# Kernel optimization log

Measured on AMD Instinct MI355X. Metric: run time of the kernel, lower is better.

## Reference

```python
import jax, jax.numpy as jnp
import numpy as np

DIM_H = 384
EPS = 0.5
HID = 768
NN = 3   # num_normal_labels (B,I,O)
NL = 7   # num_labels (O, B/I x POS/NEG/NEU)


def _make_w_trans():
    # ote_vocab: B=0, I=1, O=2 ; ts_vocab: O=0, B-POS=1, B-NEG=2, B-NEU=3, I-POS=4, I-NEG=5, I-NEU=6
    W = np.zeros((NN, NL), dtype=np.float32)
    W[0, 1] = W[0, 2] = W[0, 3] = 1.0 / 3.0  # B -> B-*
    W[1, 4] = W[1, 5] = W[1, 6] = 1.0 / 3.0  # I -> I-*
    W[2, 0] = 1.0                            # O -> O
    return jnp.asarray(W)


def setup_inputs() -> dict:
    key = jax.random.key(0)
    ks = jax.random.split(key, 16)
    B, S = 32, 512
    s = 0.02
    inp = {
        'x': jax.random.normal(ks[0], (B, S, HID), jnp.float32),
        'attention_mask': jnp.ones((B, S), jnp.int32),
        'labels': jax.random.randint(ks[1], (B, S), 0, NL, jnp.int32),
        'labels_normal': jax.random.randint(ks[2], (B, S), 0, NN, jnp.int32),
        'W_fc_normal': jax.random.normal(ks[3], (HID, NN), jnp.float32) * s,
        'b_fc_normal': jnp.zeros((NN,), jnp.float32),
        'w_ih_f': jax.random.normal(ks[4], (4 * DIM_H, HID), jnp.float32) * s,
        'w_hh_f': jax.random.normal(ks[5], (4 * DIM_H, DIM_H), jnp.float32) * s,
        'b_f': jnp.zeros((4 * DIM_H,), jnp.float32),
        'w_ih_b': jax.random.normal(ks[6], (4 * DIM_H, HID), jnp.float32) * s,
        'w_hh_b': jax.random.normal(ks[7], (4 * DIM_H, DIM_H), jnp.float32) * s,
        'b_b': jnp.zeros((4 * DIM_H,), jnp.float32),
        'W_gate': jax.random.uniform(ks[8], (2 * DIM_H, 2 * DIM_H), jnp.float32, -0.2, 0.2),
        'W_fc_upper': jax.random.normal(ks[9], (2 * DIM_H, NL), jnp.float32) * s,
        'b_fc_upper': jnp.zeros((NL,), jnp.float32),
        'W_trans': _make_w_trans(),
    }
    return inp


def _lstm_dir(xs, w_ih, w_hh, b):
    # xs: [S, B, HID] time-major; PyTorch gate order i,f,g,o
    B = xs.shape[1]
    pre = jnp.einsum('sbh,gh->sbg', xs, w_ih) + b  # precompute input projections

    def step(carry, p_t):
        h, c = carry
        g = p_t + h @ w_hh.T
        i, f, gg, o = jnp.split(g, 4, axis=-1)
        c = jax.nn.sigmoid(f) * c + jax.nn.sigmoid(i) * jnp.tanh(gg)
        h = jax.nn.sigmoid(o) * jnp.tanh(c)
        return (h, c), h

    init = (jnp.zeros((B, DIM_H), xs.dtype), jnp.zeros((B, DIM_H), xs.dtype))
    _, hs = jax.lax.scan(step, init, pre)
    return hs  # [S, B, DIM_H]


def _masked_ce(logits, labels, mask):
    logp = jax.nn.log_softmax(logits, axis=-1)
    nll = -jnp.take_along_axis(logp, labels[..., None].astype(jnp.int32), axis=-1)[..., 0]
    m = mask.astype(logits.dtype)
    return jnp.sum(nll * m) / jnp.sum(m)


def reference(x, attention_mask, labels, labels_normal, W_fc_normal, b_fc_normal,
              w_ih_f, w_hh_f, b_f, w_ih_b, w_hh_b, b_b, W_gate,
              W_fc_upper, b_fc_upper, W_trans):
    z_t = x @ W_fc_normal + b_fc_normal                      # [B,S,NN]
    loss = _masked_ce(z_t, labels_normal, attention_mask)

    xs = jnp.transpose(x, (1, 0, 2))                         # [S,B,HID]
    hf = _lstm_dir(xs, w_ih_f, w_hh_f, b_f)
    hb = _lstm_dir(xs[::-1], w_ih_b, w_hh_b, b_b)[::-1]
    h_s = jnp.concatenate([hf, hb], axis=-1)                 # [S,B,2*DIM_H]

    # gated highway recurrence: gates depend only on h_s -> batched matmul + linear scan
    g = jax.nn.sigmoid(h_s @ W_gate)                         # [S,B,768]

    def gate_step(h_prev, inp):
        ht, gt = inp
        h = gt * ht + (1.0 - gt) * h_prev
        return h, h

    _, rest = jax.lax.scan(gate_step, h_s[0], (h_s[1:], g[1:]))
    h_tilde = jnp.concatenate([h_s[:1], rest], axis=0)       # [S,B,768]
    h_tilde = jnp.transpose(h_tilde, (1, 0, 2))              # [B,S,768]; dropout = identity (eval)

    z_s = h_tilde @ W_fc_upper + b_fc_upper                  # [B,S,NL]
    p = jax.nn.softmax(z_t, axis=-1)
    alpha = EPS * jnp.sum(p * p, axis=-1, keepdims=True)     # [B,S,1]
    z_s_prime = z_t @ W_trans                                # [B,S,NL]
    z_s_tilde = z_s_prime * alpha + z_s * (1.0 - alpha)

    loss = loss + _masked_ce(z_s_tilde, labels, attention_mask)
    return loss, z_s_tilde
```

## Files before the change

### kernel.cpp

```cpp
#include <hip/hip_runtime.h>

#define B_SZ   32
#define S_LEN  512
#define HID    768
#define DH     384
#define G4     1536
#define NPOS   16384
#define EPS_C  0.5f
#define NCH    24576
#define CHK    64
#define NCHK   8

typedef _Float16 h2 __attribute__((ext_vector_type(2)));
typedef short bf16x8 __attribute__((ext_vector_type(8)));
typedef float f32x4 __attribute__((ext_vector_type(4)));

static __device__ __forceinline__ float sigm(float x) { return 1.0f / (1.0f + __expf(-x)); }
static __device__ __forceinline__ float tanh_fast(float x) {
    return 1.0f - 2.0f / (__expf(2.0f * x) + 1.0f);
}

static __device__ __forceinline__ unsigned short f2bf(float f) {
    union { float f; unsigned u; } v; v.f = f;
    unsigned r = v.u + 0x7FFF + ((v.u >> 16) & 1);
    return (unsigned short)(r >> 16);
}
static __device__ __forceinline__ float bf2f(unsigned short u) {
    union { unsigned u; float f; } v; v.u = ((unsigned)u) << 16; return v.f;
}

static __device__ __forceinline__ float wred(float v) {
#pragma unroll
    for (int off = 32; off > 0; off >>= 1) v += __shfl_down(v, off, 64);
    return v;
}

static __device__ __forceinline__ float dot2acc(h2 a, h2 b, float c) {
#if __has_builtin(__builtin_amdgcn_fdot2)
    return __builtin_amdgcn_fdot2(a, b, c, false);
#else
    return c + (float)a.x * (float)b.x + (float)a.y * (float)b.y;
#endif
}

static __device__ __forceinline__ h2 hcast(unsigned u) { return __builtin_bit_cast(h2, u); }

template <int CTRL>
static __device__ __forceinline__ float dpp_shl_add(float v) {
#if __has_builtin(__builtin_amdgcn_mov_dpp)
    int o = __builtin_amdgcn_mov_dpp(__builtin_bit_cast(int, v), CTRL, 0xF, 0xF, true);
    return v + __builtin_bit_cast(float, o);
#else
    return v + __shfl_down(v, CTRL - 0x100, 64);
#endif
}
static __device__ __forceinline__ float red8(float v) {
    v = dpp_shl_add<0x101>(v);
    v = dpp_shl_add<0x102>(v);
    v = dpp_shl_add<0x104>(v);
    return v;
}

__global__ void wprep(const float* __restrict__ wf, const float* __restrict__ wb,
                      unsigned* __restrict__ wpk) {
    int gid = blockIdx.x * 256 + threadIdx.x;
    int d = (gid >= 294912) ? 1 : 0;
    int j = gid - d * 294912;
    const float* src = d ? wb : wf;
    _Float16 a = (_Float16)src[2 * j];
    _Float16 b = (_Float16)src[2 * j + 1];
    unsigned pa = __builtin_bit_cast(unsigned short, a);
    unsigned pb = __builtin_bit_cast(unsigned short, b);
    wpk[(size_t)d * 294912 + j] = pa | (pb << 16);
}

__global__ __launch_bounds__(256) void cast_bf16(
    const float* __restrict__ src, unsigned short* __restrict__ dst, int n4) {
    int i = blockIdx.x * 256 + threadIdx.x;
    if (i >= n4) return;
    float4 v = *(const float4*)(src + (size_t)i * 4);
    ushort4 o;
    o.x = f2bf(v.x); o.y = f2bf(v.y); o.z = f2bf(v.z); o.w = f2bf(v.w);
    *(ushort4*)(dst + (size_t)i * 4) = o;
}

__global__ __launch_bounds__(256) void wgt_prep(
    const float* __restrict__ Wg, unsigned short* __restrict__ Wgt) {
    int i = blockIdx.x * 256 + threadIdx.x;
    int k = i / 768, n = i - k * 768;
    Wgt[(size_t)n * 768 + k] = f2bf(Wg[i]);
}

__global__ __launch_bounds__(256) void zt_kernel(
    const float* __restrict__ x, const int* __restrict__ amask,
    const int* __restrict__ labn, const float* __restrict__ Wfc,
    const float* __restrict__ bfc, const float* __restrict__ Wtr,
    float* __restrict__ alpha, float* __restrict__ zsp,
    float* __restrict__ p0, float* __restrict__ p2) {
    const int gid  = blockIdx.x * blockDim.x + threadIdx.x;
    const int pos  = gid >> 6, lane = gid & 63, wv = threadIdx.x >> 6;
    __shared__ float r0[4], r2[4];
    const float* xp = x + (size_t)pos * HID;
    float a0 = 0.f, a1 = 0.f, a2 = 0.f;
#pragma unroll
    for (int j = 0; j < 12; ++j) {
        int k = lane + (j << 6);
        float xv = xp[k];
        a0 += xv * Wfc[k * 3 + 0];
        a1 += xv * Wfc[k * 3 + 1];
        a2 += xv * Wfc[k * 3 + 2];
    }
    a0 = wred(a0); a1 = wred(a1); a2 = wred(a2);
    if (lane == 0) {
        float z0 = a0 + bfc[0], z1 = a1 + bfc[1], z2 = a2 + bfc[2];
        float mx = fmaxf(z0, fmaxf(z1, z2));
        float e0 = __expf(z0 - mx), e1 = __expf(z1 - mx), e2 = __expf(z2 - mx);
        float se = e0 + e1 + e2;
        float m  = (float)amask[pos];
        int  lab = labn[pos];
        float zl = (lab == 0) ? z0 : ((lab == 1) ? z1 : z2);
        r0[wv] = (mx + __logf(se) - zl) * m;
        r2[wv] = m;
        float q0 = e0 / se, q1 = e1 / se, q2 = e2 / se;
        alpha[pos] = EPS_C * (q0 * q0 + q1 * q1 + q2 * q2);
#pragma unroll
        for (int cc = 0; cc < 7; ++cc)
            zsp[(size_t)pos * 7 + cc] = z0 * Wtr[cc] + z1 * Wtr[7 + cc] + z2 * Wtr[14 + cc];
    }
    __syncthreads();
    if (threadIdx.x == 0) {
        p0[blockIdx.x] = r0[0] + r0[1] + r0[2] + r0[3];
        p2[blockIdx.x] = r2[0] + r2[1] + r2[2] + r2[3];
    }
}

__global__ __launch_bounds__(256) void gemm_mfma(
    const unsigned short* __restrict__ A, const unsigned short* __restrict__ B,
    const float* __restrict__ bias, void* __restrict__ Cout,
    int M, int N, int K, int mode) {
    __shared__ __align__(16) unsigned short As[128][40];
    __shared__ __align__(16) unsigned short Bs[128][40];
    const int tid = threadIdx.x;
    const int m0 = blockIdx.y * 128, n0 = blockIdx.x * 128;
    const int wave = tid >> 6, lane = tid & 63;
    const int wm = (wave & 1) * 64, wn = (wave >> 1) * 64;
    const int lm = lane & 15, quad = lane >> 4;
    f32x4 acc[4][4] = {};

    for (int k0 = 0; k0 < K; k0 += 32) {
#pragma unroll
        for (int r = 0; r < 2; ++r) {
            int seg = tid + r * 256;
            int row = seg >> 2, c16 = (seg & 3) << 3;
            uint4 va = *(const uint4*)(A + (size_t)(m0 + row) * K + k0 + c16);
            *(uint4*)&As[row][c16] = va;
            uint4 vb = *(const uint4*)(B + (size_t)(n0 + row) * K + k0 + c16);
            *(uint4*)&Bs[row][c16] = vb;
        }
        __syncthreads();
        bf16x8 af[4], bfr[4];
#pragma unroll
        for (int i = 0; i < 4; ++i) {
            af[i]  = *(const bf16x8*)&As[wm + i * 16 + lm][quad * 8];
            bfr[i] = *(const bf16x8*)&Bs[wn + i * 16 + lm][quad * 8];
        }
#pragma unroll
        for (int mi = 0; mi < 4; ++mi)
#pragma unroll
            for (int ni = 0; ni < 4; ++ni)
                acc[mi][ni] = __builtin_amdgcn_mfma_f32_16x16x32_bf16(
                    af[mi], bfr[ni], acc[mi][ni], 0, 0, 0);
        __syncthreads();
    }

    const int rbase = quad * 4;
#pragma unroll
    for (int mi = 0; mi < 4; ++mi) {
#pragma unroll
        for (int ni = 0; ni < 4; ++ni) {
            const int col = n0 + wn + ni * 16 + lm;
            const float bv = (mode == 0) ? bias[col] : 0.0f;
#pragma unroll
            for (int r = 0; r < 4; ++r) {
                const int row = m0 + wm + mi * 16 + rbase + r;
                float v = acc[mi][ni][r];
                if (mode == 0)
                    ((unsigned short*)Cout)[(size_t)row * N + col] = f2bf(v + bv);
                else
                    ((unsigned short*)Cout)[(size_t)row * N + col] = f2bf(sigm(v));
            }
        }
    }
}

#define DOT8(W, H, A0, A1) { \
    A0 = dot2acc(hcast(W.x), hcast(H.x), A0); \
    A1 = dot2acc(hcast(W.y), hcast(H.y), A1); \
    A0 = dot2acc(hcast(W.z), hcast(H.z), A0); \
    A1 = dot2acc(hcast(W.w), hcast(H.w), A1); }

__global__ __launch_bounds__(768)
__attribute__((amdgpu_waves_per_eu(3, 3)))
void lstm_scan10(
    const unsigned* __restrict__ wpk,
    const unsigned short* __restrict__ pre,
    unsigned short* __restrict__ h_sb,
    unsigned long long* __restrict__ hx64) {
    const int blk   = blockIdx.x;
    const int chain = blk & 63;
    const int rp    = blk >> 6;
    const int d = chain >> 5, b = chain & 31;
    const int tid = threadIdx.x;
    const int u = tid >> 3;
    const int p = tid & 7;
    const int base = rp * 96;
    const int G0 = base + u;

    __shared__ __align__(16) _Float16 lh16[2][384];

    const uint4* wq = (const uint4*)wpk + ((size_t)d * 1536 + G0) * 48 + p * 6;
    const uint4 wi0 = wq[0],         wi1 = wq[1],         wi2 = wq[2],
                wi3 = wq[3],         wi4 = wq[4],         wi5 = wq[5];
    const uint4 wf0 = wq[18432],     wf1 = wq[18433],     wf2 = wq[18434],
                wf3 = wq[18435],     wf4 = wq[18436],     wf5 = wq[18437];
    const uint4 wg0 = wq[36864],     wg1 = wq[36865],     wg2 = wq[36866],
                wg3 = wq[36867],     wg4 = wq[36868],     wg5 = wq[36869];
    const uint4 wo0 = wq[55296],     wo1 = wq[55297],     wo2 = wq[55298],
                wo3 = wq[55299],     wo4 = wq[55300],     wo5 = wq[55301];

    const unsigned short* prb =
        pre + ((size_t)d * B_SZ + b) * S_LEN * G4 + G0 + (p & 3) * 384;

    float c = 0.0f;

    for (int s = 0; s < S_LEN; ++s) {
        const int t  = d ? (S_LEN - 1 - s) : s;
        const int lb = s & 1;
        float prev = 0.0f;
        if (p < 4) prev = bf2f(prb[(size_t)t * G4]);

        if (s == 0) {
            if (tid < 384) lh16[0][tid] = (_Float16)0.0f;
        } else if (tid < 288) {
            const int uu = tid + (tid >= base ? 96 : 0);
            const unsigned long long* srcp =
                hx64 + ((size_t)((s - 1) & 1) * 64 + chain) * 384 + uu;
            unsigned long long v =
                __hip_atomic_load(srcp, __ATOMIC_RELAXED, __HIP_MEMORY_SCOPE_AGENT);
            while ((unsigned)(v >> 32) != (unsigned)(s - 1)) {
                __builtin_amdgcn_s_sleep(1);
                v = __hip_atomic_load(srcp, __ATOMIC_RELAXED, __HIP_MEMORY_SCOPE_AGENT);
            }
            lh16[lb][uu] = (_Float16)__builtin_bit_cast(float, (unsigned)v);
        }
        __syncthreads();

        {
            const uint4* hq = (const uint4*)&lh16[lb][0] + p * 6;
            const uint4 h0 = hq[0], h1 = hq[1], h2 = hq[2],
                        h3 = hq[3], h4 = hq[4], h5 = hq[5];
            float i0 = 0.f, i1 = 0.f, f0 = 0.f, f1 = 0.f;
            float g0 = 0.f, g1 = 0.f, o0 = 0.f, o1 = 0.f;
            DOT8(wi0, h0, i0, i1) DOT8(wi1, h1, i0, i1) DOT8(wi2, h2, i0, i1)
            DOT8(wi3, h3, i0, i1) DOT8(wi4, h4, i0, i1) DOT8(wi5, h5, i0, i1)
            DOT8(wf0, h0, f0, f1) DOT8(wf1, h1, f0, f1) DOT8(wf2, h2, f0, f1)
            DOT8(wf3, h3, f0, f1) DOT8(wf4, h4, f0, f1) DOT8(wf5, h5, f0, f1)
            DOT8(wg0, h0, g0, g1) DOT8(wg1, h1, g0, g1) DOT8(wg2, h2, g0, g1)
            DOT8(wg3, h3, g0, g1) DOT8(wg4, h4, g0, g1) DOT8(wg5, h5, g0, g1)
            DOT8(wo0, h0, o0, o1) DOT8(wo1, h1, o0, o1) DOT8(wo2, h2, o0, o1)
            DOT8(wo3, h3, o0, o1) DOT8(wo4, h4, o0, o1) DOT8(wo5, h5, o0, o1)
            float gi = i0 + i1, gf = f0 + f1, gg = g0 + g1, go = o0 + o1;
            if      (p == 0) gi += prev;
            else if (p == 1) gf += prev;
            else if (p == 2) gg += prev;
            else if (p == 3) go += prev;
            gi = red8(gi); gf = red8(gf); gg = red8(gg); go = red8(go);

            if (p == 0) {
                c = sigm(gf) * c + sigm(gi) * tanh_fast(gg);
                float h = sigm(go) * tanh_fast(c);
                unsigned long long v = ((unsigned long long)(unsigned)s << 32)
                                     | (unsigned long long)__builtin_bit_cast(unsigned, h);
                __hip_atomic_store(hx64 + ((size_t)lb * 64 + chain) * 384 + G0,
                                   v, __ATOMIC_RELAXED, __HIP_MEMORY_SCOPE_AGENT);
                h_sb[((size_t)t * B_SZ + b) * HID + d * DH + G0] = f2bf(h);
                lh16[lb ^ 1][G0] = (_Float16)h;
            }
        }
    }
}

__global__ __launch_bounds__(256) void gscanA(
    const unsigned short* __restrict__ g, const unsigned short* __restrict__ hsb,
    float2* __restrict__ ab) {
    int id = blockIdx.x * 256 + threadIdx.x;
    int chunk = id / NCH, chain = id - chunk * NCH;
    int t0 = chunk * CHK;
    float A = 1.f, Bv = 0.f;
    for (int i = 0; i < CHK; ++i) {
        int t = t0 + i;
        size_t idx = (size_t)t * NCH + chain;
        float gv = bf2f(g[idx]);
        float hv = bf2f(hsb[idx]);
        float a = (t == 0) ? 0.f : (1.f - gv);
        float bb = (t == 0) ? hv : gv * hv;
        A  = a * A;
        Bv = a * Bv + bb;
    }
    ab[id] = make_float2(A, Bv);
}

__global__ __launch_bounds__(256) void gscanB(
    const float2* __restrict__ ab, float* __restrict__ cin) {
    int chain = blockIdx.x * 256 + threadIdx.x;
    float h = 0.f;
#pragma unroll
    for (int j = 0; j < NCHK; ++j) {
        cin[(size_t)j * NCH + chain] = h;
        float2 t = ab[(size_t)j * NCH + chain];
        h = t.x * h + t.y;
    }
}

__global__ __launch_bounds__(256) void gscanC(
    const unsigned short* __restrict__ g, unsigned short* __restrict__ hsb,
    const float* __restrict__ cin) {
    int id = blockIdx.x * 256 + threadIdx.x;
    int chunk = id / NCH, chain = id - chunk * NCH;
    int t0 = chunk * CHK;
    float h = cin[(size_t)chunk * NCH + chain];
    for (int i = 0; i < CHK; ++i) {
        int t = t0 + i;
        size_t idx = (size_t)t * NCH + chain;
        float gv = bf2f(g[idx]);
        float v  = bf2f(hsb[idx]);
        h = (t == 0) ? v : (gv * v + (1.f - gv) * h);
        hsb[idx] = f2bf(h);
    }
}

__global__ __launch_bounds__(256) void final_k(
    const unsigned short* __restrict__ ht, const float* __restrict__ Wup,
    const float* __restrict__ bup, const float* __restrict__ alpha,
    const float* __restrict__ zsp, const int* __restrict__ labels,
    const int* __restrict__ amask, float* __restrict__ out, float* __restrict__ p1) {
    const int gid = blockIdx.x * blockDim.x + threadIdx.x;
    const int pos = gid >> 6, lane = gid & 63, wv = threadIdx.x >> 6;
    __shared__ float r1[4];
    const int bb = pos >> 9, tt = pos & 511;
    const unsigned short* hp = ht + (size_t)tt * (B_SZ * HID) + (size_t)bb * HID;
    float acc[7] = {};
#pragma unroll
    for (int j = 0; j < 12; ++j) {
        int k = lane + (j << 6);
        float hv = bf2f(hp[k]);
        const float* wr = Wup + k * 7;
#pragma unroll
        for (int cc = 0; cc < 7; ++cc) acc[cc] += hv * wr[cc];
    }
#pragma unroll
    for (int cc = 0; cc < 7; ++cc) acc[cc] = wred(acc[cc]);
    if (lane == 0) {
        float al = alpha[pos];
        float z[7], mx = -1e30f;
#pragma unroll
        for (int cc = 0; cc < 7; ++cc) {
            float v = acc[cc] + bup[cc];
            v = zsp[(size_t)pos * 7 + cc] * al + v * (1.0f - al);
            z[cc] = v;
            mx = fmaxf(mx, v);
            out[1 + (size_t)pos * 7 + cc] = v;
        }
        float se = 0.f;
#pragma unroll
        for (int cc = 0; cc < 7; ++cc) se += __expf(z[cc] - mx);
        float lse = mx + __logf(se);
        int lab = labels[pos];
        float zl = z[0];
#pragma unroll
        for (int cc = 1; cc < 7; ++cc) if (lab == cc) zl = z[cc];
        float m = (float)amask[pos];
        r1[wv] = (lse - zl) * m;
    }
    __syncthreads();
    if (threadIdx.x == 0)
        p1[blockIdx.x] = r1[0] + r1[1] + r1[2] + r1[3];
}

__global__ __launch_bounds__(256) void loss_k(
    const float* __restrict__ p0, const float* __restrict__ p1,
    const float* __restrict__ p2, float* __restrict__ out) {
    const int tid = threadIdx.x, lane = tid & 63, wv = tid >> 6;
    __shared__ float rs[4][3];
    float s0 = 0.f, s1 = 0.f, s2 = 0.f;
    for (int i = tid; i < 4096; i += 256) {
        s0 += p0[i]; s1 += p1[i]; s2 += p2[i];
    }
    s0 = wred(s0); s1 = wred(s1); s2 = wred(s2);
    if (lane == 0) { rs[wv][0] = s0; rs[wv][1] = s1; rs[wv][2] = s2; }
    __syncthreads();
    if (tid == 0) {
        float t0 = rs[0][0] + rs[1][0] + rs[2][0] + rs[3][0];
        float t1 = rs[0][1] + rs[1][1] + rs[2][1] + rs[3][1];
        float t2 = rs[0][2] + rs[1][2] + rs[2][2] + rs[3][2];
        out[0] = t0 / t2 + t1 / t2;
    }
}

extern "C" void kernel_launch(void* const* d_in, const int* in_sizes, int n_in,
                              void* d_out, int out_size, void* d_ws, size_t ws_size,
                              hipStream_t stream) {
    const float* x     = (const float*)d_in[0];
    const int*   amask = (const int*)d_in[1];
    const int*   labels= (const int*)d_in[2];
    const int*   labn  = (const int*)d_in[3];
    const float* Wfc   = (const float*)d_in[4];
    const float* bfc   = (const float*)d_in[5];
    const float* wihf  = (const float*)d_in[6];
    const float* whhf  = (const float*)d_in[7];
    const float* bf    = (const float*)d_in[8];
    const float* wihb  = (const float*)d_in[9];
    const float* whhb  = (const float*)d_in[10];
    const float* bb    = (const float*)d_in[11];
    const float* Wg    = (const float*)d_in[12];
    const float* Wup   = (const float*)d_in[13];
    const float* bup   = (const float*)d_in[14];
    const float* Wtr   = (const float*)d_in[15];
    float* out = (float*)d_out;
    (void)in_sizes; (void)n_in; (void)out_size; (void)ws_size;

    char* ws = (char*)d_ws;
    size_t off = 0;
    auto alloc = [&](size_t bytes) -> char* {
        char* p = ws + off;
        off = (off + bytes + 255) & ~(size_t)255;
        return p;
    };
    unsigned* w16buf    = (unsigned*)alloc((size_t)2 * 1536 * 192 * 4);
    unsigned short* pre = (unsigned short*)alloc((size_t)2 * NPOS * G4 * 2);
    unsigned short* xb  = (unsigned short*)alloc((size_t)NPOS * HID * 2);
    unsigned short* wfb = (unsigned short*)alloc((size_t)G4 * HID * 2);
    unsigned short* wbb = (unsigned short*)alloc((size_t)G4 * HID * 2);
    unsigned short* wgt = (unsigned short*)alloc((size_t)HID * HID * 2);
    float* alpha        = (float*)alloc((size_t)NPOS * 4);
    float* zsp          = (float*)alloc((size_t)NPOS * 7 * 4);
    unsigned long long* hx64 = (unsigned long long*)alloc((size_t)2 * 64 * 384 * 8);
    float2* ab          = (float2*)alloc((size_t)NCHK * NCH * 8);
    float* cin          = (float*)alloc((size_t)NCHK * NCH * 4);
    float* part0        = (float*)alloc(4096 * 4);
    float* part1        = (float*)alloc(4096 * 4);
    float* part2        = (float*)alloc(4096 * 4);
    unsigned short* gbuf = (unsigned short*)pre;
    unsigned short* h_sb = xb;


    wprep<<<2304, 256, 0, stream>>>(whhf, whhb, w16buf);
    cast_bf16<<<12288, 256, 0, stream>>>(x, xb, NPOS * HID / 4);
    cast_bf16<<<1152, 256, 0, stream>>>(wihf, wfb, G4 * HID / 4);
    cast_bf16<<<1152, 256, 0, stream>>>(wihb, wbb, G4 * HID / 4);
    wgt_prep<<<2304, 256, 0, stream>>>(Wg, wgt);

    zt_kernel<<<4096, 256, 0, stream>>>(x, amask, labn, Wfc, bfc, Wtr, alpha, zsp,
                                        part0, part2);

    gemm_mfma<<<dim3(12, 128), 256, 0, stream>>>(xb, wfb, bf, pre, NPOS, G4, HID, 0);
    gemm_mfma<<<dim3(12, 128), 256, 0, stream>>>(xb, wbb, bb, pre + (size_t)NPOS * G4,
                                                 NPOS, G4, HID, 0);

    lstm_scan10<<<256, 768, 0, stream>>>(w16buf, pre, h_sb, hx64);

    gemm_mfma<<<dim3(6, 128), 256, 0, stream>>>(h_sb, wgt, nullptr, gbuf, NPOS, HID, HID, 1);

    gscanA<<<768, 256, 0, stream>>>(gbuf, h_sb, ab);
    gscanB<<<96, 256, 0, stream>>>(ab, cin);
    gscanC<<<768, 256, 0, stream>>>(gbuf, h_sb, cin);

    final_k<<<4096, 256, 0, stream>>>(h_sb, Wup, bup, alpha, zsp, labels, amask, out, part1);

    loss_k<<<1, 256, 0, stream>>>(part0, part1, part2, out);
}
```

Before: 1.376 ms.

## Process two batch chains per LSTM scan block to reuse register-held weights

Each persistent LSTM scan block now handles two batch chains (b and b+16) in the same direction, so the recurrent weights held in registers serve two hidden-state dot products per step. The grid shrinks from 256 to 128 blocks, and all 768 threads take part in the hidden-state exchange and pre-activation loads. This halves the number of blocks spinning on cross-block flags and doubles arithmetic per weight load. In exchange, each step does twice the serial dot-product work per block, which may lengthen the per-step critical path.

```diff
diff --git a/kernel.cpp b/kernel.cpp
--- a/kernel.cpp
+++ b/kernel.cpp
@@ -201,22 +201,25 @@
 
 __global__ __launch_bounds__(768)
 __attribute__((amdgpu_waves_per_eu(3, 3)))
-void lstm_scan10(
+void lstm_scan11(
     const unsigned* __restrict__ wpk,
     const unsigned short* __restrict__ pre,
     unsigned short* __restrict__ h_sb,
     unsigned long long* __restrict__ hx64) {
-    const int blk   = blockIdx.x;
-    const int chain = blk & 63;
-    const int rp    = blk >> 6;
-    const int d = chain >> 5, b = chain & 31;
+    const int blk  = blockIdx.x;
+    const int pair = blk & 31;
+    const int rp   = blk >> 5;
+    const int d  = pair >> 4;
+    const int bb = pair & 15;
+    const int b0 = bb, b1 = bb + 16;
+    const int c0 = d * 32 + b0, c1 = d * 32 + b1;
     const int tid = threadIdx.x;
     const int u = tid >> 3;
     const int p = tid & 7;
     const int base = rp * 96;
     const int G0 = base + u;
 
-    __shared__ __align__(16) _Float16 lh16[2][384];
+    __shared__ __align__(16) _Float16 lh16[2][2][384];
 
     const uint4* wq = (const uint4*)wpk + ((size_t)d * 1536 + G0) * 48 + p * 6;
     const uint4 wi0 = wq[0],         wi1 = wq[1],         wi2 = wq[2],
@@ -228,64 +231,98 @@
     const uint4 wo0 = wq[55296],     wo1 = wq[55297],     wo2 = wq[55298],
                 wo3 = wq[55299],     wo4 = wq[55300],     wo5 = wq[55301];
 
+    const int pb = (p < 4) ? b0 : b1;
     const unsigned short* prb =
-        pre + ((size_t)d * B_SZ + b) * S_LEN * G4 + G0 + (p & 3) * 384;
-
-    float c = 0.0f;
+        pre + ((size_t)d * B_SZ + pb) * S_LEN * G4 + G0 + (p & 3) * 384;
+
+    const int sc = (tid >= 384) ? 1 : 0;
+    const int st = tid - sc * 384;
+    const int sch = sc ? c1 : c0;
+
+    float cs0 = 0.0f, cs1 = 0.0f;
 
     for (int s = 0; s < S_LEN; ++s) {
         const int t  = d ? (S_LEN - 1 - s) : s;
         const int lb = s & 1;
-        float prev = 0.0f;
-        if (p < 4) prev = bf2f(prb[(size_t)t * G4]);
+        float prev = bf2f(prb[(size_t)t * G4]);
 
         if (s == 0) {
-            if (tid < 384) lh16[0][tid] = (_Float16)0.0f;
-        } else if (tid < 288) {
-            const int uu = tid + (tid >= base ? 96 : 0);
+            lh16[0][sc][st] = (_Float16)0.0f;
+        } else if (st < 288) {
+            const int uu = st + (st >= base ? 96 : 0);
             const unsigned long long* srcp =
-                hx64 + ((size_t)((s - 1) & 1) * 64 + chain) * 384 + uu;
+                hx64 + ((size_t)((s - 1) & 1) * 64 + sch) * 384 + uu;
             unsigned long long v =
                 __hip_atomic_load(srcp, __ATOMIC_RELAXED, __HIP_MEMORY_SCOPE_AGENT);
             while ((unsigned)(v >> 32) != (unsigned)(s - 1)) {
                 __builtin_amdgcn_s_sleep(1);
                 v = __hip_atomic_load(srcp, __ATOMIC_RELAXED, __HIP_MEMORY_SCOPE_AGENT);
             }
-            lh16[lb][uu] = (_Float16)__builtin_bit_cast(float, (unsigned)v);
+            lh16[lb][sc][uu] = (_Float16)__builtin_bit_cast(float, (unsigned)v);
         }
         __syncthreads();
 
+        float gi0, gf0, gg0, go0, gi1, gf1, gg1, go1;
         {
-            const uint4* hq = (const uint4*)&lh16[lb][0] + p * 6;
-            const uint4 h0 = hq[0], h1 = hq[1], h2 = hq[2],
-                        h3 = hq[3], h4 = hq[4], h5 = hq[5];
+            const uint4* hq0 = (const uint4*)&lh16[lb][0][0] + p * 6;
+            const uint4 h00 = hq0[0], h01 = hq0[1], h02 = hq0[2],
+                        h03 = hq0[3], h04 = hq0[4], h05 = hq0[5];
             float i0 = 0.f, i1 = 0.f, f0 = 0.f, f1 = 0.f;
             float g0 = 0.f, g1 = 0.f, o0 = 0.f, o1 = 0.f;
-            DOT8(wi0, h0, i0, i1) DOT8(wi1, h1, i0, i1) DOT8(wi2, h2, i0, i1)
-            DOT8(wi3, h3, i0, i1) DOT8(wi4, h4, i0, i1) DOT8(wi5, h5, i0, i1)
-            DOT8(wf0, h0, f0, f1) DOT8(wf1, h1, f0, f1) DOT8(wf2, h2, f0, f1)
-            DOT8(wf3, h3, f0, f1) DOT8(wf4, h4, f0, f1) DOT8(wf5, h5, f0, f1)
-            DOT8(wg0, h0, g0, g1) DOT8(wg1, h1, g0, g1) DOT8(wg2, h2, g0, g1)
-            DOT8(wg3, h3, g0, g1) DOT8(wg4, h4, g0, g1) DOT8(wg5, h5, g0, g1)
-            DOT8(wo0, h0, o0, o1) DOT8(wo1, h1, o0, o1) DOT8(wo2, h2, o0, o1)
-            DOT8(wo3, h3, o0, o1) DOT8(wo4, h4, o0, o1) DOT8(wo5, h5, o0, o1)
-            float gi = i0 + i1, gf = f0 + f1, gg = g0 + g1, go = o0 + o1;
-            if      (p == 0) gi += prev;
-            else if (p == 1) gf += prev;
-            else if (p == 2) gg += prev;
-            else if (p == 3) go += prev;
-            gi = red8(gi); gf = red8(gf); gg = red8(gg); go = red8(go);
-
-            if (p == 0) {
-                c = sigm(gf) * c + sigm(gi) * tanh_fast(gg);
-                float h = sigm(go) * tanh_fast(c);
-                unsigned long long v = ((unsigned long long)(unsigned)s << 32)
-                                     | (unsigned long long)__builtin_bit_cast(unsigned, h);
-                __hip_atomic_store(hx64 + ((size_t)lb * 64 + chain) * 384 + G0,
-                                   v, __ATOMIC_RELAXED, __HIP_MEMORY_SCOPE_AGENT);
-                h_sb[((size_t)t * B_SZ + b) * HID + d * DH + G0] = f2bf(h);
-                lh16[lb ^ 1][G0] = (_Float16)h;
-            }
+            DOT8(wi0, h00, i0, i1) DOT8(wi1, h01, i0, i1) DOT8(wi2, h02, i0, i1)
+            DOT8(wi3, h03, i0, i1) DOT8(wi4, h04, i0, i1) DOT8(wi5, h05, i0, i1)
+            DOT8(wf0, h00, f0, f1) DOT8(wf1, h01, f0, f1) DOT8(wf2, h02, f0, f1)
+            DOT8(wf3, h03, f0, f1) DOT8(wf4, h04, f0, f1) DOT8(wf5, h05, f0, f1)
+            DOT8(wg0, h00, g0, g1) DOT8(wg1, h01, g0, g1) DOT8(wg2, h02, g0, g1)
+            DOT8(wg3, h03, g0, g1) DOT8(wg4, h04, g0, g1) DOT8(wg5, h05, g0, g1)
+            DOT8(wo0, h00, o0, o1) DOT8(wo1, h01, o0, o1) DOT8(wo2, h02, o0, o1)
+            DOT8(wo3, h03, o0, o1) DOT8(wo4, h04, o0, o1) DOT8(wo5, h05, o0, o1)
+            gi0 = i0 + i1; gf0 = f0 + f1; gg0 = g0 + g1; go0 = o0 + o1;
+        }
+        {
+            const uint4* hq1 = (const uint4*)&lh16[lb][1][0] + p * 6;
+            const uint4 h10 = hq1[0], h11 = hq1[1], h12 = hq1[2],
+                        h13 = hq1[3], h14 = hq1[4], h15 = hq1[5];
+            float i0 = 0.f, i1 = 0.f, f0 = 0.f, f1 = 0.f;
+            float g0 = 0.f, g1 = 0.f, o0 = 0.f, o1 = 0.f;
+            DOT8(wi0, h10, i0, i1) DOT8(wi1, h11, i0, i1) DOT8(wi2, h12, i0, i1)
+            DOT8(wi3, h13, i0, i1) DOT8(wi4, h14, i0, i1) DOT8(wi5, h15, i0, i1)
+            DOT8(wf0, h10, f0, f1) DOT8(wf1, h11, f0, f1) DOT8(wf2, h12, f0, f1)
+            DOT8(wf3, h13, f0, f1) DOT8(wf4, h14, f0, f1) DOT8(wf5, h15, f0, f1)
+            DOT8(wg0, h10, g0, g1) DOT8(wg1, h11, g0, g1) DOT8(wg2, h12, g0, g1)
+            DOT8(wg3, h13, g0, g1) DOT8(wg4, h14, g0, g1) DOT8(wg5, h15, g0, g1)
+            DOT8(wo0, h10, o0, o1) DOT8(wo1, h11, o0, o1) DOT8(wo2, h12, o0, o1)
+            DOT8(wo3, h13, o0, o1) DOT8(wo4, h14, o0, o1) DOT8(wo5, h15, o0, o1)
+            gi1 = i0 + i1; gf1 = f0 + f1; gg1 = g0 + g1; go1 = o0 + o1;
+        }
+        if      (p == 0) gi0 += prev;
+        else if (p == 1) gf0 += prev;
+        else if (p == 2) gg0 += prev;
+        else if (p == 3) go0 += prev;
+        else if (p == 4) gi1 += prev;
+        else if (p == 5) gf1 += prev;
+        else if (p == 6) gg1 += prev;
+        else             go1 += prev;
+        gi0 = red8(gi0); gf0 = red8(gf0); gg0 = red8(gg0); go0 = red8(go0);
+        gi1 = red8(gi1); gf1 = red8(gf1); gg1 = red8(gg1); go1 = red8(go1);
+
+        if (p == 0) {
+            cs0 = sigm(gf0) * cs0 + sigm(gi0) * tanh_fast(gg0);
+            float h0 = sigm(go0) * tanh_fast(cs0);
+            cs1 = sigm(gf1) * cs1 + sigm(gi1) * tanh_fast(gg1);
+            float h1 = sigm(go1) * tanh_fast(cs1);
+            unsigned long long v0 = ((unsigned long long)(unsigned)s << 32)
+                                  | (unsigned long long)__builtin_bit_cast(unsigned, h0);
+            unsigned long long v1 = ((unsigned long long)(unsigned)s << 32)
+                                  | (unsigned long long)__builtin_bit_cast(unsigned, h1);
+            __hip_atomic_store(hx64 + ((size_t)lb * 64 + c0) * 384 + G0,
+                               v0, __ATOMIC_RELAXED, __HIP_MEMORY_SCOPE_AGENT);
+            __hip_atomic_store(hx64 + ((size_t)lb * 64 + c1) * 384 + G0,
+                               v1, __ATOMIC_RELAXED, __HIP_MEMORY_SCOPE_AGENT);
+            h_sb[((size_t)t * B_SZ + b0) * HID + d * DH + G0] = f2bf(h0);
+            h_sb[((size_t)t * B_SZ + b1) * HID + d * DH + G0] = f2bf(h1);
+            lh16[lb ^ 1][0][G0] = (_Float16)h0;
+            lh16[lb ^ 1][1][G0] = (_Float16)h1;
         }
     }
 }
@@ -467,7 +504,7 @@
     gemm_mfma<<<dim3(12, 128), 256, 0, stream>>>(xb, wbb, bb, pre + (size_t)NPOS * G4,
                                                  NPOS, G4, HID, 0);
 
-    lstm_scan10<<<256, 768, 0, stream>>>(w16buf, pre, h_sb, hx64);
+    lstm_scan11<<<128, 768, 0, stream>>>(w16buf, pre, h_sb, hx64);
 
     gemm_mfma<<<dim3(6, 128), 256, 0, stream>>>(h_sb, wgt, nullptr, gbuf, NPOS, HID, HID, 1);
 
```

Measured after the change: 2.092 ms. +52.0%, slower.

## Move half of LSTM recurrent weights to LDS and fuse x cast into zt_kernel

Applied to the files above, without the earlier changes.

The persistent LSTM scan kernel used to keep all four gate weight slices in registers. Now it keeps only the i and f slices there and stages the g and o slices in dynamic shared memory (about 148 KB), reading them back from LDS on every timestep. This cuts register pressure, at the price of extra LDS traffic inside the latency-critical recurrence loop. Separately, the bf16 cast of x is folded into zt_kernel, which already reads x, so one full pass over the input and one kernel launch are removed.

```diff
diff --git a/kernel.cpp b/kernel.cpp
--- a/kernel.cpp
+++ b/kernel.cpp
@@ -96,16 +96,19 @@
     const int* __restrict__ labn, const float* __restrict__ Wfc,
     const float* __restrict__ bfc, const float* __restrict__ Wtr,
     float* __restrict__ alpha, float* __restrict__ zsp,
-    float* __restrict__ p0, float* __restrict__ p2) {
+    float* __restrict__ p0, float* __restrict__ p2,
+    unsigned short* __restrict__ xb) {
     const int gid  = blockIdx.x * blockDim.x + threadIdx.x;
     const int pos  = gid >> 6, lane = gid & 63, wv = threadIdx.x >> 6;
     __shared__ float r0[4], r2[4];
     const float* xp = x + (size_t)pos * HID;
+    unsigned short* xo = xb + (size_t)pos * HID;
     float a0 = 0.f, a1 = 0.f, a2 = 0.f;
 #pragma unroll
     for (int j = 0; j < 12; ++j) {
         int k = lane + (j << 6);
         float xv = xp[k];
+        xo[k] = f2bf(xv);
         a0 += xv * Wfc[k * 3 + 0];
         a1 += xv * Wfc[k * 3 + 1];
         a2 += xv * Wfc[k * 3 + 2];
@@ -201,7 +204,7 @@
 
 __global__ __launch_bounds__(768)
 __attribute__((amdgpu_waves_per_eu(3, 3)))
-void lstm_scan10(
+void lstm_scan12(
     const unsigned* __restrict__ wpk,
     const unsigned short* __restrict__ pre,
     unsigned short* __restrict__ h_sb,
@@ -216,17 +219,21 @@
     const int base = rp * 96;
     const int G0 = base + u;
 
-    __shared__ __align__(16) _Float16 lh16[2][384];
+    extern __shared__ __align__(16) char smem[];
+    uint4*     wlds = (uint4*)smem;
+    _Float16*  lh16 = (_Float16*)(smem + 12 * 768 * 16);
 
     const uint4* wq = (const uint4*)wpk + ((size_t)d * 1536 + G0) * 48 + p * 6;
-    const uint4 wi0 = wq[0],         wi1 = wq[1],         wi2 = wq[2],
-                wi3 = wq[3],         wi4 = wq[4],         wi5 = wq[5];
-    const uint4 wf0 = wq[18432],     wf1 = wq[18433],     wf2 = wq[18434],
-                wf3 = wq[18435],     wf4 = wq[18436],     wf5 = wq[18437];
-    const uint4 wg0 = wq[36864],     wg1 = wq[36865],     wg2 = wq[36866],
-                wg3 = wq[36867],     wg4 = wq[36868],     wg5 = wq[36869];
-    const uint4 wo0 = wq[55296],     wo1 = wq[55297],     wo2 = wq[55298],
-                wo3 = wq[55299],     wo4 = wq[55300],     wo5 = wq[55301];
+    const uint4 wi0 = wq[0],     wi1 = wq[1],     wi2 = wq[2],
+                wi3 = wq[3],     wi4 = wq[4],     wi5 = wq[5];
+    const uint4 wf0 = wq[18432], wf1 = wq[18433], wf2 = wq[18434],
+                wf3 = wq[18435], wf4 = wq[18436], wf5 = wq[18437];
+
+#pragma unroll
+    for (int j = 0; j < 6; ++j) {
+        wlds[j * 768 + tid]       = wq[36864 + j];
+        wlds[(6 + j) * 768 + tid] = wq[55296 + j];
+    }
 
     const unsigned short* prb =
         pre + ((size_t)d * B_SZ + b) * S_LEN * G4 + G0 + (p & 3) * 384;
@@ -240,7 +247,7 @@
         if (p < 4) prev = bf2f(prb[(size_t)t * G4]);
 
         if (s == 0) {
-            if (tid < 384) lh16[0][tid] = (_Float16)0.0f;
+            if (tid < 384) lh16[tid] = (_Float16)0.0f;
         } else if (tid < 288) {
             const int uu = tid + (tid >= base ? 96 : 0);
             const unsigned long long* srcp =
@@ -251,24 +258,44 @@
                 __builtin_amdgcn_s_sleep(1);
                 v = __hip_atomic_load(srcp, __ATOMIC_RELAXED, __HIP_MEMORY_SCOPE_AGENT);
             }
-            lh16[lb][uu] = (_Float16)__builtin_bit_cast(float, (unsigned)v);
+            lh16[lb * 384 + uu] = (_Float16)__builtin_bit_cast(float, (unsigned)v);
         }
         __syncthreads();
 
         {
-            const uint4* hq = (const uint4*)&lh16[lb][0] + p * 6;
+            const uint4* hq = (const uint4*)(lh16 + lb * 384) + p * 6;
             const uint4 h0 = hq[0], h1 = hq[1], h2 = hq[2],
                         h3 = hq[3], h4 = hq[4], h5 = hq[5];
             float i0 = 0.f, i1 = 0.f, f0 = 0.f, f1 = 0.f;
-            float g0 = 0.f, g1 = 0.f, o0 = 0.f, o1 = 0.f;
             DOT8(wi0, h0, i0, i1) DOT8(wi1, h1, i0, i1) DOT8(wi2, h2, i0, i1)
             DOT8(wi3, h3, i0, i1) DOT8(wi4, h4, i0, i1) DOT8(wi5, h5, i0, i1)
             DOT8(wf0, h0, f0, f1) DOT8(wf1, h1, f0, f1) DOT8(wf2, h2, f0, f1)
             DOT8(wf3, h3, f0, f1) DOT8(wf4, h4, f0, f1) DOT8(wf5, h5, f0, f1)
-            DOT8(wg0, h0, g0, g1) DOT8(wg1, h1, g0, g1) DOT8(wg2, h2, g0, g1)
-            DOT8(wg3, h3, g0, g1) DOT8(wg4, h4, g0, g1) DOT8(wg5, h5, g0, g1)
-            DOT8(wo0, h0, o0, o1) DOT8(wo1, h1, o0, o1) DOT8(wo2, h2, o0, o1)
-            DOT8(wo3, h3, o0, o1) DOT8(wo4, h4, o0, o1) DOT8(wo5, h5, o0, o1)
+            float g0 = 0.f, g1 = 0.f, o0 = 0.f, o1 = 0.f;
+            {
+                const uint4 w0 = wlds[0 * 768 + tid];
+                const uint4 w1 = wlds[1 * 768 + tid];
+                const uint4 w2 = wlds[2 * 768 + tid];
+                DOT8(w0, h0, g0, g1) DOT8(w1, h1, g0, g1) DOT8(w2, h2, g0, g1)
+            }
+            {
+                const uint4 w3 = wlds[3 * 768 + tid];
+                const uint4 w4 = wlds[4 * 768 + tid];
+                const uint4 w5 = wlds[5 * 768 + tid];
+                DOT8(w3, h3, g0, g1) DOT8(w4, h4, g0, g1) DOT8(w5, h5, g0, g1)
+            }
+            {
+                const uint4 w0 = wlds[6 * 768 + tid];
+                const uint4 w1 = wlds[7 * 768 + tid];
+                const uint4 w2 = wlds[8 * 768 + tid];
+                DOT8(w0, h0, o0, o1) DOT8(w1, h1, o0, o1) DOT8(w2, h2, o0, o1)
+            }
+            {
+                const uint4 w3 = wlds[9 * 768 + tid];
+                const uint4 w4 = wlds[10 * 768 + tid];
+                const uint4 w5 = wlds[11 * 768 + tid];
+                DOT8(w3, h3, o0, o1) DOT8(w4, h4, o0, o1) DOT8(w5, h5, o0, o1)
+            }
             float gi = i0 + i1, gf = f0 + f1, gg = g0 + g1, go = o0 + o1;
             if      (p == 0) gi += prev;
             else if (p == 1) gf += prev;
@@ -284,7 +311,7 @@
                 __hip_atomic_store(hx64 + ((size_t)lb * 64 + chain) * 384 + G0,
                                    v, __ATOMIC_RELAXED, __HIP_MEMORY_SCOPE_AGENT);
                 h_sb[((size_t)t * B_SZ + b) * HID + d * DH + G0] = f2bf(h);
-                lh16[lb ^ 1][G0] = (_Float16)h;
+                lh16[(lb ^ 1) * 384 + G0] = (_Float16)h;
             }
         }
     }
@@ -428,6 +455,14 @@
     const float* Wtr   = (const float*)d_in[15];
     float* out = (float*)d_out;
     (void)in_sizes; (void)n_in; (void)out_size; (void)ws_size;
+
+    static bool attr_set = false;
+    if (!attr_set) {
+        hipFuncSetAttribute((const void*)lstm_scan12,
+                            hipFuncAttributeMaxDynamicSharedMemorySize,
+                            12 * 768 * 16 + 2 * 384 * 2);
+        attr_set = true;
+    }
 
     char* ws = (char*)d_ws;
     size_t off = 0;
@@ -455,19 +490,19 @@
 
 
     wprep<<<2304, 256, 0, stream>>>(whhf, whhb, w16buf);
-    cast_bf16<<<12288, 256, 0, stream>>>(x, xb, NPOS * HID / 4);
     cast_bf16<<<1152, 256, 0, stream>>>(wihf, wfb, G4 * HID / 4);
     cast_bf16<<<1152, 256, 0, stream>>>(wihb, wbb, G4 * HID / 4);
     wgt_prep<<<2304, 256, 0, stream>>>(Wg, wgt);
 
     zt_kernel<<<4096, 256, 0, stream>>>(x, amask, labn, Wfc, bfc, Wtr, alpha, zsp,
-                                        part0, part2);
+                                        part0, part2, xb);
 
     gemm_mfma<<<dim3(12, 128), 256, 0, stream>>>(xb, wfb, bf, pre, NPOS, G4, HID, 0);
     gemm_mfma<<<dim3(12, 128), 256, 0, stream>>>(xb, wbb, bb, pre + (size_t)NPOS * G4,
                                                  NPOS, G4, HID, 0);
 
-    lstm_scan10<<<256, 768, 0, stream>>>(w16buf, pre, h_sb, hx64);
+    lstm_scan12<<<256, 768, 12 * 768 * 16 + 2 * 384 * 2, stream>>>(
+        w16buf, pre, h_sb, hx64);
 
     gemm_mfma<<<dim3(6, 128), 256, 0, stream>>>(h_sb, wgt, nullptr, gbuf, NPOS, HID, HID, 1);
 
```

Result: slower. 1.436 ms (+4.4%).
